# Optimization experiments

Measured on AMD Instinct MI355X. Metric: run time of the kernel, lower is better.

Reference implementation:

```python
import jax, jax.numpy as jnp
import numpy as np

NQ = 4
NL = 3
HEADS = 8

_H = jnp.asarray(np.array([[1, 1], [1, -1]], np.complex64) / np.sqrt(2.0))
_X = jnp.asarray(np.array([[0, 1], [1, 0]], np.complex64))
_Y = jnp.asarray(np.array([[0, -1j], [1j, 0]], np.complex64))
_Z = jnp.asarray(np.array([[1, 0], [0, -1]], np.complex64))
_CNOT = jnp.asarray(np.array([[1, 0, 0, 0], [0, 1, 0, 0], [0, 0, 0, 1], [0, 0, 1, 0]], np.complex64))


def _rx(t):
    c = jnp.cos(t / 2).astype(jnp.complex64)
    s = (-1j * jnp.sin(t / 2)).astype(jnp.complex64)
    return jnp.stack([jnp.stack([c, s]), jnp.stack([s, c])])


def _ry(t):
    c = jnp.cos(t / 2).astype(jnp.complex64)
    s = jnp.sin(t / 2).astype(jnp.complex64)
    return jnp.stack([jnp.stack([c, -s]), jnp.stack([s, c])])


def _rz(t):
    e = jnp.exp((-0.5j) * t).astype(jnp.complex64)
    z = jnp.zeros((), jnp.complex64)
    return jnp.stack([jnp.stack([e, z]), jnp.stack([z, jnp.conj(e)])])


def _crx(t):
    # control-RX in |control,target> basis
    return jnp.eye(4, dtype=jnp.complex64).at[2:, 2:].set(_rx(t))


def _ap1(psi, U, q):
    # apply 2x2 gate U on qubit axis q of psi:(2,2,2,2)
    return jnp.moveaxis(jnp.tensordot(U, psi, axes=[[1], [q]]), 0, q)


def _ap2(psi, U, q1, q2):
    p = jnp.moveaxis(psi, (q1, q2), (0, 1)).reshape(4, 4)
    p = (U @ p).reshape(2, 2, 2, 2)
    return jnp.moveaxis(p, (0, 1), (q1, q2))


def _expv(psi, P, q):
    return jnp.real(jnp.vdot(psi, _ap1(psi, P, q)))


def _circuit(inp, w, ew, gam, bet):
    # inp:(4,)  w,ew:(3,4)  gam,bet:(3,)  -> (12,) expvals Z,X,Y
    psi = jnp.zeros((16,), jnp.complex64).at[0].set(1.0).reshape(2, 2, 2, 2)
    for i in range(NQ):  # AngleEmbedding(rotation='Y')
        psi = _ap1(psi, _ry(inp[i]), i)
    for L in range(NL):
        for i in range(NQ):
            psi = _ap1(psi, _rx(w[L, i]), i)
            psi = _ap1(psi, _ry(w[L, i]), i)
            psi = _ap1(psi, _rz(w[L, i]), i)
        for i in range(NQ):  # CRX entangling ring
            psi = _ap2(psi, _crx(ew[L, i]), i, (i + 1) % NQ)
        # Grover diffusion
        for q in range(NQ):
            psi = _ap1(psi, _H, q)
        for q in range(NQ):
            psi = _ap1(psi, _X, q)
        psi = _ap1(psi, _H, NQ - 1)
        psi = psi.at[1, 1, 1, :].set(psi[1, 1, 1, ::-1])  # CCCX ctrl=[0,1,2] tgt=3
        psi = _ap1(psi, _H, NQ - 1)
        for q in range(NQ):
            psi = _ap1(psi, _X, q)
        for q in range(NQ):
            psi = _ap1(psi, _H, q)
        # QAOA cost + mixer
        for i in range(NQ - 1):
            psi = _ap2(psi, _CNOT, i, i + 1)
            psi = _ap1(psi, _rz(gam[L]), i + 1)
            psi = _ap2(psi, _CNOT, i, i + 1)
        for q in range(NQ):
            psi = _ap1(psi, _rx(bet[L]), q)
    meas = [_expv(psi, _Z, q) for q in range(NQ)]
    meas += [_expv(psi, _X, q) for q in range(NQ)]
    meas += [_expv(psi, _Y, q) for q in range(NQ)]
    return jnp.stack(meas)


_vqc = jax.vmap(_circuit, in_axes=(0, None, None, None, None))


def _layernorm(x, g, b, eps=1e-5):
    mu = jnp.mean(x, -1, keepdims=True)
    var = jnp.mean((x - mu) ** 2, -1, keepdims=True)
    return (x - mu) * jax.lax.rsqrt(var + eps) * g + b


def _qtransform(xf, Wp, bp, ln_g, ln_b, w, ew, gam, bet):
    p = jnp.tanh(xf @ Wp.T + bp)  # (BS,4)
    p = _layernorm(p, ln_g, ln_b)
    return _vqc(p, w, ew, gam, bet)  # (BS,12)


def setup_inputs() -> dict:
    key = jax.random.key(0)
    ks = jax.random.split(key, 32)
    B, S, Hd = 4, 1024, 512
    d = {"x": jax.random.normal(ks[0], (B, S, Hd), jnp.float32)}
    d["Wp"] = jax.random.normal(ks[1], (NQ, Hd), jnp.float32) * 0.05
    d["bp"] = jnp.zeros((NQ,), jnp.float32)
    d["ln_g"] = jnp.ones((NQ,), jnp.float32)
    d["ln_b"] = jnp.zeros((NQ,), jnp.float32)
    i = 2
    for pfx in ["q", "k", "v"]:
        d[pfx + "w"] = 0.01 * jax.random.normal(ks[i], (NL, NQ), jnp.float32)
        d[pfx + "e"] = 0.01 * jax.random.normal(ks[i + 1], (NL, NQ), jnp.float32)
        d[pfx + "g"] = 0.01 * jax.random.normal(ks[i + 2], (NL,), jnp.float32)
        d[pfx + "b"] = 0.01 * jax.random.normal(ks[i + 3], (NL,), jnp.float32)
        i += 4
    fused = 3 * NQ
    d["Wq"] = jax.random.normal(ks[i], (Hd, fused), jnp.float32) * 0.2
    d["bq"] = jnp.zeros((Hd,), jnp.float32)
    d["Wk"] = jax.random.normal(ks[i + 1], (Hd, fused), jnp.float32) * 0.2
    d["bk"] = jnp.zeros((Hd,), jnp.float32)
    d["Wv"] = jax.random.normal(ks[i + 2], (Hd, fused), jnp.float32) * 0.2
    d["bv"] = jnp.zeros((Hd,), jnp.float32)
    d["Wo"] = jax.random.normal(ks[i + 3], (Hd, Hd), jnp.float32) * 0.05
    d["bo"] = jnp.zeros((Hd,), jnp.float32)
    return d


def reference(x, Wp, bp, ln_g, ln_b, qw, qe, qg, qb, kw, ke, kg, kb, vw, ve, vg, vb,
              Wq, bq, Wk, bk, Wv, bv, Wo, bo):
    B, S, Hd = x.shape
    hd = Hd // HEADS
    xf = x.reshape(B * S, Hd)
    tq = _qtransform(xf, Wp, bp, ln_g, ln_b, qw, qe, qg, qb)
    tk = _qtransform(xf, Wp, bp, ln_g, ln_b, kw, ke, kg, kb)
    tv = _qtransform(xf, Wp, bp, ln_g, ln_b, vw, ve, vg, vb)
    q = (tq @ Wq.T + bq).reshape(B, S, HEADS, hd)
    k = (tk @ Wk.T + bk).reshape(B, S, HEADS, hd)
    v = (tv @ Wv.T + bv).reshape(B, S, HEADS, hd)
    scale = float(hd) ** 0.5
    attn = jax.nn.softmax(jnp.einsum('bqhd,bkhd->bhqk', q, k) / scale, axis=-1)
    out = jnp.einsum('bhqk,bkhd->bqhd', attn, v).reshape(B, S, Hd)
    return out @ Wo.T + bo
```

## Files before the change

kernel.cpp:

```cpp
#include <hip/hip_runtime.h>
#include <hip/hip_bf16.h>
#include <math.h>

#define NROWS 4096
#define HD 512
#define HEADS 8
#define HDD 64
#define SEQ 1024
#define QSCALE 0.18033688011112042f

typedef unsigned short u16;
typedef unsigned int u32;
typedef unsigned long long u64;
typedef __attribute__((ext_vector_type(8))) short sh8;
typedef __attribute__((ext_vector_type(4))) float f4;

__device__ __forceinline__ f4 mfma16(sh8 a, sh8 b, f4 c) {
  return __builtin_amdgcn_mfma_f32_16x16x32_bf16(a, b, c, 0, 0, 0);
}

__device__ __forceinline__ u16 f2bf(float x) {
  union { float f; unsigned u; } v; v.f = x;
  unsigned r = v.u + 0x7fff + ((v.u >> 16) & 1);
  return (u16)(r >> 16);
}

#define SWZA(r, cb) ((((r) * 128) + (cb)) ^ (((r) & 7) << 4))
#define SWZB(r, cb) ((((r) * 256) + (cb)) ^ (((r) & 7) << 4))

__global__ __launch_bounds__(256) void k_prep(
    const float* __restrict__ qw, const float* __restrict__ qe,
    const float* __restrict__ qg, const float* __restrict__ qb,
    const float* __restrict__ kw, const float* __restrict__ ke,
    const float* __restrict__ kg, const float* __restrict__ kb,
    const float* __restrict__ vw, const float* __restrict__ ve,
    const float* __restrict__ vg, const float* __restrict__ vb,
    float* __restrict__ Mout) {
  const int c = blockIdx.x;
  const int tid = threadIdx.x;
  __shared__ float aC[32], aS[32];
  __shared__ float GT[60][8];
  __shared__ int   GM[60][2];
  __shared__ float PF[3][16][2];
  __shared__ float SR[16][17], SI[16][17];
  __shared__ float TS[16], TI[16];
  __shared__ float Ur[256], Ui[256];

  const float* w = (c == 0) ? qw : (c == 1) ? kw : vw;
  const float* e = (c == 0) ? qe : (c == 1) ? ke : ve;
  const float* g = (c == 0) ? qg : (c == 1) ? kg : vg;
  const float* b = (c == 0) ? qb : (c == 1) ? kb : vb;

  if (tid < 30) {
    float ang = (tid < 12) ? w[tid] : (tid < 24) ? e[tid - 12]
               : (tid < 27) ? g[tid - 24] : b[tid - 27];
    float s_, c_;
    sincosf(0.5f * ang, &s_, &c_);
    aC[tid] = c_; aS[tid] = s_;
  }
  __syncthreads();

  if (tid < 60) {
    int L = tid / 20, s5 = tid % 20;
    int typ, aidx, M, C;
    if (s5 < 12) {
      int q = s5 / 3; typ = s5 % 3; aidx = L * 4 + q; M = 8 >> q; C = 0;
    } else if (s5 < 16) {
      int q = s5 - 12; typ = 0; aidx = 12 + L * 4 + q;
      C = 8 >> q; M = 8 >> ((q + 1) & 3);
    } else {
      int q = s5 - 16; typ = 0; aidx = 27 + L; M = 8 >> q; C = 0;
    }
    float cc = aC[aidx], ss = aS[aidx];
    float u0r = cc, u0i = 0.f, u1r = 0.f, u1i = 0.f,
          u2r = 0.f, u2i = 0.f, u3r = cc, u3i = 0.f;
    if (typ == 0)      { u1i = -ss; u2i = -ss; }
    else if (typ == 1) { u1r = -ss; u2r = ss; }
    else               { u0i = -ss; u3i = ss; }
    GT[tid][0] = u0r; GT[tid][1] = u0i; GT[tid][2] = u1r; GT[tid][3] = u1i;
    GT[tid][4] = u2r; GT[tid][5] = u2i; GT[tid][6] = u3r; GT[tid][7] = u3i;
    GM[tid][0] = M; GM[tid][1] = C;
  }
  if (tid >= 64 && tid < 112) {
    int idx = tid - 64, L = idx >> 4, a = idx & 15;
    float cg = aC[24 + L], sg = aS[24 + L];
    float c2 = cg * cg - sg * sg, s2 = 2.f * cg * sg;
    float c3 = cg * c2 - sg * s2, s3 = cg * s2 + sg * c2;
    int u = (a ^ (a >> 1)) & 7;
    int n = (u & 1) + ((u >> 1) & 1) + ((u >> 2) & 1);
    PF[L][a][0] = (n == 0 || n == 3) ? c3 : cg;
    PF[L][a][1] = (n == 0) ? -s3 : (n == 1) ? -sg : (n == 2) ? sg : s3;
  }
  for (int i = tid; i < 256; i += 256) {
    SR[i >> 4][i & 15] = (i >> 4) == (i & 15) ? 1.f : 0.f;
    SI[i >> 4][i & 15] = 0.f;
  }
  __syncthreads();

  const int p = tid >> 4, col = tid & 15;
  for (int L = 0; L < 3; ++L) {
    for (int s5 = 0; s5 < 16; ++s5) {
      if (tid < 128) {
        int gi = L * 20 + s5;
        const float* u = GT[gi];
        int M = GM[gi][0], C = GM[gi][1];
        int lo = p & (M - 1);
        int a = ((p - lo) << 1) | lo;
        int bb = a | M;
        bool act = (C == 0) | ((a & C) != 0);
        float ar = SR[a][col], ai = SI[a][col];
        float br = SR[bb][col], bi = SI[bb][col];
        float nar = u[0]*ar - u[1]*ai + u[2]*br - u[3]*bi;
        float nai = u[0]*ai + u[1]*ar + u[2]*bi + u[3]*br;
        float nbr = u[4]*ar - u[5]*ai + u[6]*br - u[7]*bi;
        float nbi = u[4]*ai + u[5]*ar + u[6]*bi + u[7]*br;
        SR[a][col]  = act ? nar : ar;  SI[a][col]  = act ? nai : ai;
        SR[bb][col] = act ? nbr : br;  SI[bb][col] = act ? nbi : bi;
      }
      __syncthreads();
    }
    if (tid < 16) {
      float sR = 0.f, sI = 0.f;
      for (int a = 0; a < 16; ++a) { sR += SR[a][tid]; sI += SI[a][tid]; }
      TS[tid] = sR * 0.125f; TI[tid] = sI * 0.125f;
    }
    __syncthreads();
    if (tid < 128) {
      for (int k = 0; k < 2; ++k) {
        int a = 2 * p + k;
        float vr = SR[a][col] - TS[col];
        float vi = SI[a][col] - TI[col];
        float pc = PF[L][a][0], ps = PF[L][a][1];
        SR[a][col] = vr * pc - vi * ps;
        SI[a][col] = vr * ps + vi * pc;
      }
    }
    __syncthreads();
    for (int s5 = 16; s5 < 20; ++s5) {
      if (tid < 128) {
        int gi = L * 20 + s5;
        const float* u = GT[gi];
        int M = GM[gi][0];
        int lo = p & (M - 1);
        int a = ((p - lo) << 1) | lo;
        int bb = a | M;
        float ar = SR[a][col], ai = SI[a][col];
        float br = SR[bb][col], bi = SI[bb][col];
        SR[a][col]  = u[0]*ar - u[1]*ai + u[2]*br - u[3]*bi;
        SI[a][col]  = u[0]*ai + u[1]*ar + u[2]*bi + u[3]*br;
        SR[bb][col] = u[4]*ar - u[5]*ai + u[6]*br - u[7]*bi;
        SI[bb][col] = u[4]*ai + u[5]*ar + u[6]*bi + u[7]*br;
      }
      __syncthreads();
    }
  }

  for (int i = tid; i < 256; i += 256) {
    Ur[i] = SR[i >> 4][i & 15];
    Ui[i] = SI[i >> 4][i & 15];
  }
  __syncthreads();

  if (tid < 192) {
    const int j = tid >> 4, a = tid & 15;
    const int typ = j >> 2;
    const int Mm = 8 >> (j & 3);
    float ax[4] = {0.f,0.f,0.f,0.f}, ay[4] = {0.f,0.f,0.f,0.f},
          az[4] = {0.f,0.f,0.f,0.f}, aw[4] = {0.f,0.f,0.f,0.f};
#pragma clang loop unroll_count(4)
    for (int k = 0; k < 16; ++k) {
      float uar = Ur[k * 16 + a], uai = Ui[k * 16 + a];
      int k2; float cR, cI;
      if (typ == 0)      { k2 = k;      float z = (k & Mm) ? -1.f : 1.f; cR = z*uar; cI = z*uai; }
      else if (typ == 1) { k2 = k ^ Mm; cR = uar; cI = uai; }
      else               { k2 = k ^ Mm; float sg = (k & Mm) ? 1.f : -1.f; cR = sg*uai; cI = -sg*uar; }
      const float* ur2 = Ur + k2 * 16;
      const float* ui2 = Ui + k2 * 16;
#pragma unroll
      for (int i = 0; i < 4; ++i) {
        ax[i] += cR * ur2[i*4+0] + cI * ui2[i*4+0];
        ay[i] += cR * ur2[i*4+1] + cI * ui2[i*4+1];
        az[i] += cR * ur2[i*4+2] + cI * ui2[i*4+2];
        aw[i] += cR * ur2[i*4+3] + cI * ui2[i*4+3];
      }
    }
    float* dst = Mout + ((c * 12 + j) * 16 + a) * 16;
#pragma unroll
    for (int i = 0; i < 4; ++i)
      ((float4*)dst)[i] = make_float4(ax[i], ay[i], az[i], aw[i]);
  }
}

__global__ __launch_bounds__(256) void k_front(const float* __restrict__ x,
    const float* __restrict__ Wp, const float* __restrict__ bp,
    const float* __restrict__ ln_g, const float* __restrict__ ln_b,
    const float* __restrict__ Mg,
    const float* __restrict__ Wq, const float* __restrict__ bq,
    const float* __restrict__ Wk, const float* __restrict__ bk,
    const float* __restrict__ Wv, const float* __restrict__ bv,
    u16* __restrict__ Qo, u16* __restrict__ Ko, u16* __restrict__ Vto) {
  const int rb = blockIdx.x;
  const int tid = threadIdx.x;
  const int w = tid >> 6, lane = tid & 63;
  __shared__ float pl[4][4];
  __shared__ float psil[4][16];
  __shared__ float tt[3][4][12];

  {
    const float* xr = x + (rb * 4 + w) * HD + lane * 8;
    float4 xa = *(const float4*)xr, xb = *(const float4*)(xr + 4);
    float acc[4];
#pragma unroll
    for (int j = 0; j < 4; ++j) {
      const float* wr = Wp + j * HD + lane * 8;
      float4 wa = *(const float4*)wr, wb = *(const float4*)(wr + 4);
      acc[j] = xa.x*wa.x + xa.y*wa.y + xa.z*wa.z + xa.w*wa.w
             + xb.x*wb.x + xb.y*wb.y + xb.z*wb.z + xb.w*wb.w;
    }
#pragma unroll
    for (int j = 0; j < 4; ++j)
#pragma unroll
      for (int off = 32; off >= 1; off >>= 1)
        acc[j] += __shfl_xor(acc[j], off);
    if (lane == 0) {
      float v0 = tanhf(acc[0] + bp[0]);
      float v1 = tanhf(acc[1] + bp[1]);
      float v2 = tanhf(acc[2] + bp[2]);
      float v3 = tanhf(acc[3] + bp[3]);
      float mu = 0.25f * (v0 + v1 + v2 + v3);
      float d0 = v0 - mu, d1 = v1 - mu, d2 = v2 - mu, d3 = v3 - mu;
      float inv = rsqrtf(0.25f * (d0*d0 + d1*d1 + d2*d2 + d3*d3) + 1e-5f);
      pl[w][0] = d0 * inv * ln_g[0] + ln_b[0];
      pl[w][1] = d1 * inv * ln_g[1] + ln_b[1];
      pl[w][2] = d2 * inv * ln_g[2] + ln_b[2];
      pl[w][3] = d3 * inv * ln_g[3] + ln_b[3];
    }
  }
  __syncthreads();

  if (tid < 4) {
    float cs[4], sn[4];
    sincosf(0.5f * pl[tid][0], &sn[0], &cs[0]);
    sincosf(0.5f * pl[tid][1], &sn[1], &cs[1]);
    sincosf(0.5f * pl[tid][2], &sn[2], &cs[2]);
    sincosf(0.5f * pl[tid][3], &sn[3], &cs[3]);
    float q01[4] = {cs[0]*cs[1], cs[0]*sn[1], sn[0]*cs[1], sn[0]*sn[1]};
    float q23[4] = {cs[2]*cs[3], cs[2]*sn[3], sn[2]*cs[3], sn[2]*sn[3]};
#pragma unroll
    for (int a = 0; a < 16; ++a) psil[tid][a] = q01[a >> 2] * q23[a & 3];
  }
  __syncthreads();

  if (tid < 144) {
    const int c = tid / 48, rem = tid - c * 48, j = rem >> 2, r = rem & 3;
    float psi[16];
#pragma unroll
    for (int a = 0; a < 16; ++a) psi[a] = psil[r][a];
    const float4* Mj = (const float4*)(Mg + (c * 12 + j) * 256);
    float y = 0.f;
#pragma unroll
    for (int a = 0; a < 16; ++a) {
      float rsum = 0.f;
#pragma unroll
      for (int i = 0; i < 4; ++i) {
        float4 m4 = Mj[a * 4 + i];
        rsum += m4.x*psi[i*4] + m4.y*psi[i*4+1] + m4.z*psi[i*4+2] + m4.w*psi[i*4+3];
      }
      y += psi[a] * rsum;
    }
    tt[c][r][j] = y;
  }
  __syncthreads();

  const int o0 = tid * 2;
  const int b = rb >> 8, ss0 = (rb & 255) * 4;
  const int h = o0 >> 6, d = o0 & 63;
#pragma unroll
  for (int c = 0; c < 3; ++c) {
    const float* W  = (c == 0) ? Wq : (c == 1) ? Wk : Wv;
    const float* bb = (c == 0) ? bq : (c == 1) ? bk : bv;
    float4 w0a = *(const float4*)(W + o0 * 12);
    float4 w0b = *(const float4*)(W + o0 * 12 + 4);
    float4 w0c = *(const float4*)(W + o0 * 12 + 8);
    float4 w1a = *(const float4*)(W + o0 * 12 + 12);
    float4 w1b = *(const float4*)(W + o0 * 12 + 16);
    float4 w1c = *(const float4*)(W + o0 * 12 + 20);
    float b0 = bb[o0], b1 = bb[o0 + 1];
    float r0[4], r1[4];
#pragma unroll
    for (int r = 0; r < 4; ++r) {
      const float* t = tt[c][r];
      r0[r] = b0 + t[0]*w0a.x + t[1]*w0a.y + t[2]*w0a.z + t[3]*w0a.w
                 + t[4]*w0b.x + t[5]*w0b.y + t[6]*w0b.z + t[7]*w0b.w
                 + t[8]*w0c.x + t[9]*w0c.y + t[10]*w0c.z + t[11]*w0c.w;
      r1[r] = b1 + t[0]*w1a.x + t[1]*w1a.y + t[2]*w1a.z + t[3]*w1a.w
                 + t[4]*w1b.x + t[5]*w1b.y + t[6]*w1b.z + t[7]*w1b.w
                 + t[8]*w1c.x + t[9]*w1c.y + t[10]*w1c.z + t[11]*w1c.w;
    }
    if (c == 0) {
      u16* qrow = Qo + ((b * HEADS + h) * SEQ + ss0) * HDD + d;
#pragma unroll
      for (int r = 0; r < 4; ++r)
        *(u32*)(qrow + r * HDD) =
            (u32)f2bf(r0[r] * QSCALE) | ((u32)f2bf(r1[r] * QSCALE) << 16);
    } else if (c == 1) {
      u16* krow = Ko + ((b * HEADS + h) * SEQ + ss0) * HDD + d;
#pragma unroll
      for (int r = 0; r < 4; ++r)
        *(u32*)(krow + r * HDD) = (u32)f2bf(r0[r]) | ((u32)f2bf(r1[r]) << 16);
    } else {
      u64 v0 = (u64)((u32)f2bf(r0[0]) | ((u32)f2bf(r0[1]) << 16)) |
               ((u64)((u32)f2bf(r0[2]) | ((u32)f2bf(r0[3]) << 16)) << 32);
      u64 v1 = (u64)((u32)f2bf(r1[0]) | ((u32)f2bf(r1[1]) << 16)) |
               ((u64)((u32)f2bf(r1[2]) | ((u32)f2bf(r1[3]) << 16)) << 32);
      *(u64*)(Vto + (b * 512 + o0) * SEQ + ss0) = v0;
      *(u64*)(Vto + (b * 512 + o0 + 1) * SEQ + ss0) = v1;
    }
  }
}

__global__ __launch_bounds__(256) void k_attn_mfma(const u16* __restrict__ Q,
    const u16* __restrict__ K, const u16* __restrict__ Vt,
    u16* __restrict__ Ob) {
  const int bh = blockIdx.y, qt = blockIdx.x;
  const int tid = threadIdx.x, w = tid >> 6, l = tid & 63;
  const int lr = l & 15, lh = l >> 4;

  __shared__ u16 Kl[2][128 * 64];
  __shared__ u16 Vl[2][64 * 128];
  __shared__ u16 Pl[4][16 * 128];

  const u16* Qb = Q + (bh * SEQ + qt * 64) * HDD;
  const u16* Kb = K + bh * SEQ * HDD;
  const u16* Vb = Vt + bh * HDD * SEQ;

  sh8 qf[2];
#pragma unroll
  for (int kk = 0; kk < 2; ++kk)
    qf[kk] = *(const sh8*)(Qb + (w * 16 + lr) * HDD + kk * 32 + lh * 8);

  f4 oacc[4];
  float lsum[4] = {0.f, 0.f, 0.f, 0.f};
#pragma unroll
  for (int n = 0; n < 4; ++n) oacc[n] = (f4){0.f, 0.f, 0.f, 0.f};

  sh8 kreg[4], vreg[4];

#define STAGE_LOAD(ch) { \
    _Pragma("unroll") \
    for (int i = 0; i < 4; ++i) { \
      int idx = i * 256 + tid; \
      kreg[i] = *(const sh8*)(Kb + ((ch) * 128 + (idx >> 3)) * HDD + (idx & 7) * 8); \
      vreg[i] = *(const sh8*)(Vb + (idx >> 4) * SEQ + (ch) * 128 + (idx & 15) * 8); \
    } }
#define STAGE_WRITE(buf) { \
    _Pragma("unroll") \
    for (int i = 0; i < 4; ++i) { \
      int idx = i * 256 + tid; \
      *(sh8*)((char*)Kl[buf] + SWZA(idx >> 3, (idx & 7) * 16)) = kreg[i]; \
      *(sh8*)((char*)Vl[buf] + SWZB(idx >> 4, (idx & 15) * 16)) = vreg[i]; \
    } }

  STAGE_LOAD(0)
  STAGE_WRITE(0)
  __syncthreads();

  for (int ch = 0; ch < SEQ / 128; ++ch) {
    const int cur = ch & 1;
    if (ch < 7) STAGE_LOAD(ch + 1)

    f4 sacc[8];
#pragma unroll
    for (int n = 0; n < 8; ++n) sacc[n] = (f4){0.f, 0.f, 0.f, 0.f};
#pragma unroll
    for (int kk = 0; kk < 2; ++kk) {
#pragma unroll
      for (int n = 0; n < 8; ++n) {
        sh8 kf = *(const sh8*)((const char*)Kl[cur] + SWZA(n * 16 + lr, kk * 64 + lh * 16));
        sacc[n] = mfma16(qf[kk], kf, sacc[n]);
      }
    }

#pragma unroll
    for (int n = 0; n < 8; ++n) {
#pragma unroll
      for (int r = 0; r < 4; ++r) {
        float pv = exp2f(sacc[n][r]);
        lsum[r] += pv;
        *(u16*)((char*)Pl[w] + SWZB(lh * 4 + r, (n * 16 + lr) * 2)) = f2bf(pv);
      }
    }

#pragma unroll
    for (int kk = 0; kk < 4; ++kk) {
      sh8 pf = *(const sh8*)((const char*)Pl[w] + SWZB(lr, kk * 64 + lh * 16));
#pragma unroll
      for (int n = 0; n < 4; ++n) {
        sh8 vf = *(const sh8*)((const char*)Vl[cur] + SWZB(n * 16 + lr, kk * 64 + lh * 16));
        oacc[n] = mfma16(pf, vf, oacc[n]);
      }
    }

    if (ch < 7) STAGE_WRITE(cur ^ 1)
    __syncthreads();
  }
#undef STAGE_LOAD
#undef STAGE_WRITE

#pragma unroll
  for (int r = 0; r < 4; ++r) {
    lsum[r] += __shfl_xor(lsum[r], 1); lsum[r] += __shfl_xor(lsum[r], 2);
    lsum[r] += __shfl_xor(lsum[r], 4); lsum[r] += __shfl_xor(lsum[r], 8);
  }

  int bb = bh >> 3, h = bh & 7;
#pragma unroll
  for (int r = 0; r < 4; ++r) {
    int row = qt * 64 + w * 16 + lh * 4 + r;
    float inv = 1.f / lsum[r];
#pragma unroll
    for (int n = 0; n < 4; ++n)
      Ob[(bb * SEQ + row) * HD + h * 64 + n * 16 + lr] = f2bf(oacc[n][r] * inv);
  }
}

__global__ __launch_bounds__(256) void k_oproj_mfma(const u16* __restrict__ A,
    const float* __restrict__ W, const float* __restrict__ bo,
    float* __restrict__ out) {
  const int nb = blockIdx.x, ob = blockIdx.y;
  const int tid = threadIdx.x, w = tid >> 6, l = tid & 63;
  const int lr = l & 15, lh = l >> 4;
  __shared__ u16 Al[64 * 64];
  __shared__ u16 Wl[64 * 64];
  f4 acc[4];
#pragma unroll
  for (int n = 0; n < 4; ++n) acc[n] = (f4){0.f, 0.f, 0.f, 0.f};
  for (int ch = 0; ch < 8; ++ch) {
    __syncthreads();
#pragma unroll
    for (int i = 0; i < 2; ++i) {
      int idx = i * 256 + tid;
      int r = idx >> 3, c8 = idx & 7;
      *(sh8*)((char*)Al + SWZA(r, c8 * 16)) =
          *(const sh8*)(A + (nb * 64 + r) * HD + ch * 64 + c8 * 8);
      const float* wp = W + (ob * 64 + r) * HD + ch * 64 + c8 * 8;
      float4 f0 = *(const float4*)wp;
      float4 f1 = *(const float4*)(wp + 4);
      sh8 wv;
      wv[0] = (short)f2bf(f0.x); wv[1] = (short)f2bf(f0.y);
      wv[2] = (short)f2bf(f0.z); wv[3] = (short)f2bf(f0.w);
      wv[4] = (short)f2bf(f1.x); wv[5] = (short)f2bf(f1.y);
      wv[6] = (short)f2bf(f1.z); wv[7] = (short)f2bf(f1.w);
      *(sh8*)((char*)Wl + SWZA(r, c8 * 16)) = wv;
    }
    __syncthreads();
#pragma unroll
    for (int kk = 0; kk < 2; ++kk) {
      sh8 af = *(const sh8*)((const char*)Al + SWZA(w * 16 + lr, kk * 64 + lh * 16));
#pragma unroll
      for (int n = 0; n < 4; ++n) {
        sh8 wf = *(const sh8*)((const char*)Wl + SWZA(n * 16 + lr, kk * 64 + lh * 16));
        acc[n] = mfma16(af, wf, acc[n]);
      }
    }
  }
#pragma unroll
  for (int r = 0; r < 4; ++r) {
    int row = nb * 64 + w * 16 + lh * 4 + r;
#pragma unroll
    for (int n = 0; n < 4; ++n) {
      int col = ob * 64 + n * 16 + lr;
      out[row * HD + col] = acc[n][r] + bo[col];
    }
  }
}

extern "C" void kernel_launch(void* const* d_in, const int* in_sizes, int n_in,
                              void* d_out, int out_size, void* d_ws, size_t ws_size,
                              hipStream_t stream) {
  const float* x    = (const float*)d_in[0];
  const float* Wp   = (const float*)d_in[1];
  const float* bp   = (const float*)d_in[2];
  const float* ln_g = (const float*)d_in[3];
  const float* ln_b = (const float*)d_in[4];
  const float* qw   = (const float*)d_in[5];
  const float* qe   = (const float*)d_in[6];
  const float* qg   = (const float*)d_in[7];
  const float* qb_  = (const float*)d_in[8];
  const float* kw   = (const float*)d_in[9];
  const float* ke   = (const float*)d_in[10];
  const float* kg   = (const float*)d_in[11];
  const float* kb_  = (const float*)d_in[12];
  const float* vw   = (const float*)d_in[13];
  const float* ve   = (const float*)d_in[14];
  const float* vg   = (const float*)d_in[15];
  const float* vb_  = (const float*)d_in[16];
  const float* Wq   = (const float*)d_in[17];
  const float* bq   = (const float*)d_in[18];
  const float* Wk   = (const float*)d_in[19];
  const float* bk   = (const float*)d_in[20];
  const float* Wv   = (const float*)d_in[21];
  const float* bv   = (const float*)d_in[22];
  const float* Wo   = (const float*)d_in[23];
  const float* bo   = (const float*)d_in[24];

  float* ws   = (float*)d_ws;
  float* Mbuf = ws;
  u16* qb  = (u16*)(Mbuf + 9216);
  u16* kb  = qb + 32 * SEQ * HDD;
  u16* vtb = kb + 32 * SEQ * HDD;
  u16* ab  = vtb + 32 * SEQ * HDD;

  k_prep<<<3, 256, 0, stream>>>(qw, qe, qg, qb_, kw, ke, kg, kb_,
                                vw, ve, vg, vb_, Mbuf);
  k_front<<<NROWS / 4, 256, 0, stream>>>(x, Wp, bp, ln_g, ln_b, Mbuf,
                                         Wq, bq, Wk, bk, Wv, bv, qb, kb, vtb);
  dim3 ga(SEQ / 64, 32);
  k_attn_mfma<<<ga, 256, 0, stream>>>(qb, kb, vtb, ab);
  dim3 go(NROWS / 64, HD / 64);
  k_oproj_mfma<<<go, 256, 0, stream>>>(ab, Wo, bo, (float*)d_out);
}
```

Measured before the change: 82.46 us.

## Split attention over key dimension and merge partials in output projection

Attention now splits the key sequence into two halves across a third grid dimension, doubling block count from 512 to 1024 to fill more CUs. Each half writes unnormalized fp32 partial outputs and row sums, and the output-projection kernel sums the two partials, normalizes and converts to bf16 while loading A. It also uses 64-key chunks with smaller LDS tiles and adds s_setprio around MFMA sections. In exchange it writes and reads extra fp32 partial traffic through global memory.

```diff
diff --git a/kernel.cpp b/kernel.cpp
--- a/kernel.cpp
+++ b/kernel.cpp
@@ -26,7 +26,6 @@
 }
 
 #define SWZA(r, cb) ((((r) * 128) + (cb)) ^ (((r) & 7) << 4))
-#define SWZB(r, cb) ((((r) * 256) + (cb)) ^ (((r) & 7) << 4))
 
 __global__ __launch_bounds__(256) void k_prep(
     const float* __restrict__ qw, const float* __restrict__ qe,
@@ -321,18 +320,19 @@
 
 __global__ __launch_bounds__(256) void k_attn_mfma(const u16* __restrict__ Q,
     const u16* __restrict__ K, const u16* __restrict__ Vt,
-    u16* __restrict__ Ob) {
-  const int bh = blockIdx.y, qt = blockIdx.x;
+    float* __restrict__ Op, float* __restrict__ Lp) {
+  const int bh = blockIdx.y, qt = blockIdx.x, ks = blockIdx.z;
   const int tid = threadIdx.x, w = tid >> 6, l = tid & 63;
   const int lr = l & 15, lh = l >> 4;
 
-  __shared__ u16 Kl[2][128 * 64];
-  __shared__ u16 Vl[2][64 * 128];
-  __shared__ u16 Pl[4][16 * 128];
+  __shared__ u16 Kl[2][64 * 64];
+  __shared__ u16 Vl[2][64 * 64];
+  __shared__ u16 Pl[4][16 * 64];
 
   const u16* Qb = Q + (bh * SEQ + qt * 64) * HDD;
   const u16* Kb = K + bh * SEQ * HDD;
   const u16* Vb = Vt + bh * HDD * SEQ;
+  const int CH0 = ks * 8;
 
   sh8 qf[2];
 #pragma unroll
@@ -344,64 +344,68 @@
 #pragma unroll
   for (int n = 0; n < 4; ++n) oacc[n] = (f4){0.f, 0.f, 0.f, 0.f};
 
-  sh8 kreg[4], vreg[4];
+  sh8 kreg[2], vreg[2];
 
 #define STAGE_LOAD(ch) { \
     _Pragma("unroll") \
-    for (int i = 0; i < 4; ++i) { \
+    for (int i = 0; i < 2; ++i) { \
       int idx = i * 256 + tid; \
-      kreg[i] = *(const sh8*)(Kb + ((ch) * 128 + (idx >> 3)) * HDD + (idx & 7) * 8); \
-      vreg[i] = *(const sh8*)(Vb + (idx >> 4) * SEQ + (ch) * 128 + (idx & 15) * 8); \
+      kreg[i] = *(const sh8*)(Kb + ((ch) * 64 + (idx >> 3)) * HDD + (idx & 7) * 8); \
+      vreg[i] = *(const sh8*)(Vb + (idx >> 3) * SEQ + (ch) * 64 + (idx & 7) * 8); \
     } }
 #define STAGE_WRITE(buf) { \
     _Pragma("unroll") \
-    for (int i = 0; i < 4; ++i) { \
+    for (int i = 0; i < 2; ++i) { \
       int idx = i * 256 + tid; \
       *(sh8*)((char*)Kl[buf] + SWZA(idx >> 3, (idx & 7) * 16)) = kreg[i]; \
-      *(sh8*)((char*)Vl[buf] + SWZB(idx >> 4, (idx & 15) * 16)) = vreg[i]; \
+      *(sh8*)((char*)Vl[buf] + SWZA(idx >> 3, (idx & 7) * 16)) = vreg[i]; \
     } }
 
-  STAGE_LOAD(0)
+  STAGE_LOAD(CH0)
   STAGE_WRITE(0)
   __syncthreads();
 
-  for (int ch = 0; ch < SEQ / 128; ++ch) {
-    const int cur = ch & 1;
-    if (ch < 7) STAGE_LOAD(ch + 1)
-
-    f4 sacc[8];
-#pragma unroll
-    for (int n = 0; n < 8; ++n) sacc[n] = (f4){0.f, 0.f, 0.f, 0.f};
+  for (int it = 0; it < 8; ++it) {
+    const int cur = it & 1;
+    if (it < 7) STAGE_LOAD(CH0 + it + 1)
+
+    f4 sacc[4];
+#pragma unroll
+    for (int n = 0; n < 4; ++n) sacc[n] = (f4){0.f, 0.f, 0.f, 0.f};
+    __builtin_amdgcn_s_setprio(1);
 #pragma unroll
     for (int kk = 0; kk < 2; ++kk) {
 #pragma unroll
-      for (int n = 0; n < 8; ++n) {
+      for (int n = 0; n < 4; ++n) {
         sh8 kf = *(const sh8*)((const char*)Kl[cur] + SWZA(n * 16 + lr, kk * 64 + lh * 16));
         sacc[n] = mfma16(qf[kk], kf, sacc[n]);
       }
     }
-
-#pragma unroll
-    for (int n = 0; n < 8; ++n) {
+    __builtin_amdgcn_s_setprio(0);
+
+#pragma unroll
+    for (int n = 0; n < 4; ++n) {
 #pragma unroll
       for (int r = 0; r < 4; ++r) {
         float pv = exp2f(sacc[n][r]);
         lsum[r] += pv;
-        *(u16*)((char*)Pl[w] + SWZB(lh * 4 + r, (n * 16 + lr) * 2)) = f2bf(pv);
-      }
-    }
-
-#pragma unroll
-    for (int kk = 0; kk < 4; ++kk) {
-      sh8 pf = *(const sh8*)((const char*)Pl[w] + SWZB(lr, kk * 64 + lh * 16));
+        *(u16*)((char*)Pl[w] + SWZA(lh * 4 + r, (n * 16 + lr) * 2)) = f2bf(pv);
+      }
+    }
+
+    __builtin_amdgcn_s_setprio(1);
+#pragma unroll
+    for (int kk = 0; kk < 2; ++kk) {
+      sh8 pf = *(const sh8*)((const char*)Pl[w] + SWZA(lr, kk * 64 + lh * 16));
 #pragma unroll
       for (int n = 0; n < 4; ++n) {
-        sh8 vf = *(const sh8*)((const char*)Vl[cur] + SWZB(n * 16 + lr, kk * 64 + lh * 16));
+        sh8 vf = *(const sh8*)((const char*)Vl[cur] + SWZA(n * 16 + lr, kk * 64 + lh * 16));
         oacc[n] = mfma16(pf, vf, oacc[n]);
       }
     }
-
-    if (ch < 7) STAGE_WRITE(cur ^ 1)
+    __builtin_amdgcn_s_setprio(0);
+
+    if (it < 7) STAGE_WRITE(cur ^ 1)
     __syncthreads();
   }
 #undef STAGE_LOAD
@@ -413,20 +417,22 @@
     lsum[r] += __shfl_xor(lsum[r], 4); lsum[r] += __shfl_xor(lsum[r], 8);
   }
 
-  int bb = bh >> 3, h = bh & 7;
+  const int bb = bh >> 3, h = bh & 7;
 #pragma unroll
   for (int r = 0; r < 4; ++r) {
     int row = qt * 64 + w * 16 + lh * 4 + r;
-    float inv = 1.f / lsum[r];
+    float* orow = Op + ((ks * NROWS + bb * SEQ + row) * HD) + h * 64;
 #pragma unroll
     for (int n = 0; n < 4; ++n)
-      Ob[(bb * SEQ + row) * HD + h * 64 + n * 16 + lr] = f2bf(oacc[n][r] * inv);
-  }
-}
-
-__global__ __launch_bounds__(256) void k_oproj_mfma(const u16* __restrict__ A,
-    const float* __restrict__ W, const float* __restrict__ bo,
-    float* __restrict__ out) {
+      orow[n * 16 + lr] = oacc[n][r];
+    if (lr == 0)
+      Lp[(ks * 32 + bh) * SEQ + row] = lsum[r];
+  }
+}
+
+__global__ __launch_bounds__(256) void k_oproj_mfma(const float* __restrict__ Op,
+    const float* __restrict__ Lp, const float* __restrict__ W,
+    const float* __restrict__ bo, float* __restrict__ out) {
   const int nb = blockIdx.x, ob = blockIdx.y;
   const int tid = threadIdx.x, w = tid >> 6, l = tid & 63;
   const int lr = l & 15, lh = l >> 4;
@@ -441,8 +447,24 @@
     for (int i = 0; i < 2; ++i) {
       int idx = i * 256 + tid;
       int r = idx >> 3, c8 = idx & 7;
-      *(sh8*)((char*)Al + SWZA(r, c8 * 16)) =
-          *(const sh8*)(A + (nb * 64 + r) * HD + ch * 64 + c8 * 8);
+      int grow = nb * 64 + r;
+      int bb = grow >> 10, srow = grow & 1023;
+      float linv = 1.f / (Lp[(bb * 8 + ch) * SEQ + srow] +
+                          Lp[(32 + bb * 8 + ch) * SEQ + srow]);
+      const float* o0 = Op + grow * HD + ch * 64 + c8 * 8;
+      const float* o1 = o0 + NROWS * HD;
+      float4 a0 = *(const float4*)o0,      a1 = *(const float4*)(o0 + 4);
+      float4 b0 = *(const float4*)o1,      b1 = *(const float4*)(o1 + 4);
+      sh8 av;
+      av[0] = (short)f2bf((a0.x + b0.x) * linv);
+      av[1] = (short)f2bf((a0.y + b0.y) * linv);
+      av[2] = (short)f2bf((a0.z + b0.z) * linv);
+      av[3] = (short)f2bf((a0.w + b0.w) * linv);
+      av[4] = (short)f2bf((a1.x + b1.x) * linv);
+      av[5] = (short)f2bf((a1.y + b1.y) * linv);
+      av[6] = (short)f2bf((a1.z + b1.z) * linv);
+      av[7] = (short)f2bf((a1.w + b1.w) * linv);
+      *(sh8*)((char*)Al + SWZA(r, c8 * 16)) = av;
       const float* wp = W + (ob * 64 + r) * HD + ch * 64 + c8 * 8;
       float4 f0 = *(const float4*)wp;
       float4 f1 = *(const float4*)(wp + 4);
@@ -509,14 +531,15 @@
   u16* qb  = (u16*)(Mbuf + 9216);
   u16* kb  = qb + 32 * SEQ * HDD;
   u16* vtb = kb + 32 * SEQ * HDD;
-  u16* ab  = vtb + 32 * SEQ * HDD;
+  float* Opart = (float*)(vtb + 32 * SEQ * HDD);
+  float* Lpart = Opart + 2 * NROWS * HD;
 
   k_prep<<<3, 256, 0, stream>>>(qw, qe, qg, qb_, kw, ke, kg, kb_,
                                 vw, ve, vg, vb_, Mbuf);
   k_front<<<NROWS / 4, 256, 0, stream>>>(x, Wp, bp, ln_g, ln_b, Mbuf,
                                          Wq, bq, Wk, bk, Wv, bv, qb, kb, vtb);
-  dim3 ga(SEQ / 64, 32);
-  k_attn_mfma<<<ga, 256, 0, stream>>>(qb, kb, vtb, ab);
+  dim3 ga(SEQ / 64, 32, 2);
+  k_attn_mfma<<<ga, 256, 0, stream>>>(qb, kb, vtb, Opart, Lpart);
   dim3 go(NROWS / 64, HD / 64);
-  k_oproj_mfma<<<go, 256, 0, stream>>>(ab, Wo, bo, (float*)d_out);
-}
+  k_oproj_mfma<<<go, 256, 0, stream>>>(Opart, Lpart, Wo, bo, (float*)d_out);
+}
```

Result: no change. 80.85 us (-2.0%).
